# Kernel optimization log

Measured on AMD Instinct MI355X. Metric: run time of the kernel, lower is better.

## Reference

```python
import jax, jax.numpy as jnp
import numpy as np

B, T, D = 8, 512, 64

def setup_inputs() -> dict:
    key = jax.random.key(0)
    kx, kw, kb = jax.random.split(key, 3)
    x = jax.random.normal(kx, (B, T, D), dtype=jnp.float32)
    W = jax.random.normal(kw, (D, D), dtype=jnp.float32) / np.sqrt(D)
    b = jax.random.normal(kb, (D,), dtype=jnp.float32) * 0.01
    return {"x": x, "W": W, "b": b}

def reference(x, W, b):
    # v = Linear(x): (B,T,D)
    v = jnp.einsum('btd,ed->bte', x, W) + b
    # pairwise diff: (B,T,T,D); softmax over feature dim D
    diff = x[:, :, None, :] - x[:, None, :, :]
    K = jax.nn.softmax(-(diff * diff), axis=-1)
    # out[b,i,j] = sum_d K[b,i,j,d] * v[b,i,d]  -> (B,T,T)
    out = jnp.einsum('bijd,bid->bij', K, v)
    return out
```

## Files before the change

### kernel.cpp

```cpp
#include <hip/hip_runtime.h>
#include <hip/hip_bf16.h>

#define BB 8
#define TT 512
#define DD 64
#define S_SCALE 1.2011224087864498f

typedef float v2f __attribute__((ext_vector_type(2)));
typedef unsigned short ushort_t;

static __device__ __forceinline__ float fast_exp2(float v) {
#if __has_builtin(__builtin_amdgcn_exp2f)
    return __builtin_amdgcn_exp2f(v);
#else
    return exp2f(v);
#endif
}
static __device__ __forceinline__ float fast_rcp(float v) {
#if __has_builtin(__builtin_amdgcn_rcpf)
    return __builtin_amdgcn_rcpf(v);
#else
    return 1.0f / v;
#endif
}
static __device__ __forceinline__ v2f pk_fma(v2f a, v2f b, v2f c) {
#if __has_builtin(__builtin_elementwise_fma)
    return __builtin_elementwise_fma(a, b, c);
#else
    return a * b + c;
#endif
}
static __device__ __forceinline__ v2f lohi(unsigned u) {
    v2f r;
    r.x = __uint_as_float(u << 16);
    r.y = __uint_as_float(u & 0xffff0000u);
    return r;
}

__global__ __launch_bounds__(256) void rbf_pre(
    const float* __restrict__ x, const float* __restrict__ W,
    const float* __restrict__ bias, float* __restrict__ vv,
    __hip_bfloat16* __restrict__ xs16, __hip_bfloat16* __restrict__ vs16)
{
    const int t = threadIdx.x;
    const int w = t >> 6, l = t & 63;
    const int row = blockIdx.x * 4 + w;
    const float* xr = x + (size_t)row * DD;
    const float* wr = W + (size_t)l * DD;
    float acc = bias[l];
    #pragma unroll
    for (int d = 0; d < DD; d += 4) {
        float4 xv = *(const float4*)(xr + d);
        float4 wv = *(const float4*)(wr + d);
        acc = fmaf(xv.x, wv.x, acc); acc = fmaf(xv.y, wv.y, acc);
        acc = fmaf(xv.z, wv.z, acc); acc = fmaf(xv.w, wv.w, acc);
    }
    vv  [(size_t)row * DD + l] = acc;
    xs16[(size_t)row * DD + l] = __float2bfloat16(xr[l] * S_SCALE);
    vs16[(size_t)row * DD + l] = __float2bfloat16(acc);
}

template <bool MIRROR>
static __device__ __forceinline__ void tile_compute(
    const float* __restrict__ xrow0, const float* __restrict__ vrow0,
    const ushort_t* xls, const ushort_t* vls,
    float* __restrict__ orow0, float* cbuf, int l, int ilocBase)
{
    v2f nr[4][2], nc[4][2], dn[4];
    #pragma unroll
    for (int r = 0; r < 4; ++r) {
        nr[r][0] = (v2f){0.f, 0.f}; nr[r][1] = (v2f){0.f, 0.f};
        nc[r][0] = (v2f){0.f, 0.f}; nc[r][1] = (v2f){0.f, 0.f};
        dn[r]    = (v2f){0.f, 0.f};
    }
    const v2f Sv = {S_SCALE, S_SCALE};

    #pragma unroll
    for (int c = 0; c < 8; ++c) {
        uint4 xjw = *(const uint4*)(xls + l * 72 + c * 8);
        uint4 vjw = *(const uint4*)(vls + l * 72 + c * 8);
        v2f xj0 = lohi(xjw.x), xj1 = lohi(xjw.y), xj2 = lohi(xjw.z), xj3 = lohi(xjw.w);
        v2f vj0 = lohi(vjw.x), vj1 = lohi(vjw.y), vj2 = lohi(vjw.z), vj3 = lohi(vjw.w);
        #pragma unroll
        for (int r = 0; r < 4; ++r) {
            float4 a0 = *(const float4*)(xrow0 + r * DD + c * 8);
            float4 a1 = *(const float4*)(xrow0 + r * DD + c * 8 + 4);
            float4 b0 = *(const float4*)(vrow0 + r * DD + c * 8);
            float4 b1 = *(const float4*)(vrow0 + r * DD + c * 8 + 4);
            v2f u0 = pk_fma((v2f){a0.x, a0.y}, Sv, -xj0);
            v2f u1 = pk_fma((v2f){a0.z, a0.w}, Sv, -xj1);
            v2f u2 = pk_fma((v2f){a1.x, a1.y}, Sv, -xj2);
            v2f u3 = pk_fma((v2f){a1.z, a1.w}, Sv, -xj3);
            u0 *= u0; u1 *= u1; u2 *= u2; u3 *= u3;
            v2f e0 = {fast_exp2(-u0.x), fast_exp2(-u0.y)};
            v2f e1 = {fast_exp2(-u1.x), fast_exp2(-u1.y)};
            v2f e2 = {fast_exp2(-u2.x), fast_exp2(-u2.y)};
            v2f e3 = {fast_exp2(-u3.x), fast_exp2(-u3.y)};
            nr[r][0] = pk_fma(e0, (v2f){b0.x, b0.y}, nr[r][0]);
            nr[r][0] = pk_fma(e1, (v2f){b0.z, b0.w}, nr[r][0]);
            nr[r][1] = pk_fma(e2, (v2f){b1.x, b1.y}, nr[r][1]);
            nr[r][1] = pk_fma(e3, (v2f){b1.z, b1.w}, nr[r][1]);
            if (MIRROR) {
                nc[r][0] = pk_fma(e0, vj0, nc[r][0]);
                nc[r][0] = pk_fma(e1, vj1, nc[r][0]);
                nc[r][1] = pk_fma(e2, vj2, nc[r][1]);
                nc[r][1] = pk_fma(e3, vj3, nc[r][1]);
            }
            dn[r] += (e0 + e1) + (e2 + e3);
        }
    }

    #pragma unroll
    for (int r = 0; r < 4; ++r) {
        float rd = fast_rcp(dn[r].x + dn[r].y);
        v2f sr = nr[r][0] + nr[r][1];
        orow0[(size_t)r * TT + l] = (sr.x + sr.y) * rd;
        if (MIRROR) {
            v2f sc = nc[r][0] + nc[r][1];
            cbuf[l * 20 + ilocBase + r] = (sc.x + sc.y) * rd;
        }
    }
}

__global__ __launch_bounds__(256, 4) void rbf_sym(
    const float* __restrict__ x, const float* __restrict__ vv,
    const __hip_bfloat16* __restrict__ xs16, const __hip_bfloat16* __restrict__ vs16,
    float* __restrict__ out)
{
    const int bid = blockIdx.x;
    const int b = bid / 144;
    int idx = bid - b * 144;
    int st, jt, isA;
    if (idx < 32) { jt = idx >> 2; st = 4 * jt + (idx & 3); isA = 0; }
    else {
        int k = idx - 32, tt = 1;
        while (k >= 4 * tt) { k -= 4 * tt; ++tt; }
        jt = tt; st = k; isA = 1;
    }
    const int i0 = st * 16, j0 = jt * 64;

    const int tid = threadIdx.x;
    const int w = tid >> 6, l = tid & 63;
    const int wau = __builtin_amdgcn_readfirstlane(w);

    __shared__ ushort_t xls[64 * 72];
    __shared__ ushort_t vls[64 * 72];
    __shared__ float    cbuf[64 * 20];

    {
        const uint4* xsrc = (const uint4*)(xs16 + ((size_t)b * TT + j0) * DD);
        const uint4* vsrc = (const uint4*)(vs16 + ((size_t)b * TT + j0) * DD);
        #pragma unroll
        for (int u = 0; u < 2; ++u) {
            int g = u * 256 + tid;
            int r = g >> 3, c8 = g & 7;
            *(uint4*)(xls + r * 72 + c8 * 8) = xsrc[g];
            *(uint4*)(vls + r * 72 + c8 * 8) = vsrc[g];
        }
    }
    __syncthreads();

    const int ib = b * TT + i0 + wau * 4;
    const float* xrow0 = x  + (size_t)ib * DD;
    const float* vrow0 = vv + (size_t)ib * DD;
    float* outb  = out + (size_t)b * TT * TT;
    float* orow0 = outb + (size_t)(i0 + wau * 4) * TT + j0;

    if (isA) tile_compute<true >(xrow0, vrow0, xls, vls, orow0, cbuf, l, wau * 4);
    else     tile_compute<false>(xrow0, vrow0, xls, vls, orow0, cbuf, l, wau * 4);

    __syncthreads();
    if (isA) {
        int j = tid >> 2, qf = (tid & 3) * 4;
        float4 cv = *(const float4*)(cbuf + j * 20 + qf);
        *(float4*)(outb + (size_t)(j0 + j) * TT + i0 + qf) = cv;
    }
}

extern "C" void kernel_launch(void* const* d_in, const int* in_sizes, int n_in,
                              void* d_out, int out_size, void* d_ws, size_t ws_size,
                              hipStream_t stream) {
    const float* x    = (const float*)d_in[0];
    const float* W    = (const float*)d_in[1];
    const float* bias = (const float*)d_in[2];
    float* out        = (float*)d_out;

    float* vv             = (float*)d_ws;
    __hip_bfloat16* xs16  = (__hip_bfloat16*)((char*)d_ws + (1 << 20));
    __hip_bfloat16* vs16  = (__hip_bfloat16*)((char*)d_ws + (3 << 19));

    rbf_pre<<<BB * TT / 4, 256, 0, stream>>>(x, W, bias, vv, xs16, vs16);
    rbf_sym<<<BB * 144, 256, 0, stream>>>(x, vv, xs16, vs16, out);
}
```

Before: 89.51 us.

## Stage i-rows in LDS as fp16 and drop fp32 x/v global reads

Switches the precomputed scaled x and v copies from bf16 to fp16 and stops writing or reading the fp32 v buffer. The i-side rows (x pre-scaled, v) are now loaded once per block into shared memory as fp16 instead of being read per wave from global fp32 arrays. The inner loop becomes a plain subtract, because the scale is already folded in. This cuts global/L2 traffic and the per-row scale FMA, at the cost of fp16 conversions for the i operands and some reduced precision on the i side.

```diff
diff --git a/kernel.cpp b/kernel.cpp
--- a/kernel.cpp
+++ b/kernel.cpp
@@ -1,5 +1,4 @@
 #include <hip/hip_runtime.h>
-#include <hip/hip_bf16.h>
 
 #define BB 8
 #define TT 512
@@ -7,7 +6,8 @@
 #define S_SCALE 1.2011224087864498f
 
 typedef float v2f __attribute__((ext_vector_type(2)));
-typedef unsigned short ushort_t;
+typedef float f8  __attribute__((ext_vector_type(8)));
+typedef _Float16 h8 __attribute__((ext_vector_type(8)));
 
 static __device__ __forceinline__ float fast_exp2(float v) {
 #if __has_builtin(__builtin_amdgcn_exp2f)
@@ -30,17 +30,11 @@
     return a * b + c;
 #endif
 }
-static __device__ __forceinline__ v2f lohi(unsigned u) {
-    v2f r;
-    r.x = __uint_as_float(u << 16);
-    r.y = __uint_as_float(u & 0xffff0000u);
-    return r;
-}
 
 __global__ __launch_bounds__(256) void rbf_pre(
     const float* __restrict__ x, const float* __restrict__ W,
-    const float* __restrict__ bias, float* __restrict__ vv,
-    __hip_bfloat16* __restrict__ xs16, __hip_bfloat16* __restrict__ vs16)
+    const float* __restrict__ bias,
+    _Float16* __restrict__ xh, _Float16* __restrict__ vh)
 {
     const int t = threadIdx.x;
     const int w = t >> 6, l = t & 63;
@@ -55,16 +49,15 @@
         acc = fmaf(xv.x, wv.x, acc); acc = fmaf(xv.y, wv.y, acc);
         acc = fmaf(xv.z, wv.z, acc); acc = fmaf(xv.w, wv.w, acc);
     }
-    vv  [(size_t)row * DD + l] = acc;
-    xs16[(size_t)row * DD + l] = __float2bfloat16(xr[l] * S_SCALE);
-    vs16[(size_t)row * DD + l] = __float2bfloat16(acc);
+    xh[(size_t)row * DD + l] = (_Float16)(xr[l] * S_SCALE);
+    vh[(size_t)row * DD + l] = (_Float16)acc;
 }
 
 template <bool MIRROR>
 static __device__ __forceinline__ void tile_compute(
-    const float* __restrict__ xrow0, const float* __restrict__ vrow0,
-    const ushort_t* xls, const ushort_t* vls,
-    float* __restrict__ orow0, float* cbuf, int l, int ilocBase)
+    const _Float16* xls, const _Float16* vls,
+    const _Float16* xis, const _Float16* vis,
+    float* __restrict__ orow0, float* cbuf, int l, int wau)
 {
     v2f nr[4][2], nc[4][2], dn[4];
     #pragma unroll
@@ -73,40 +66,32 @@
         nc[r][0] = (v2f){0.f, 0.f}; nc[r][1] = (v2f){0.f, 0.f};
         dn[r]    = (v2f){0.f, 0.f};
     }
-    const v2f Sv = {S_SCALE, S_SCALE};
 
     #pragma unroll
     for (int c = 0; c < 8; ++c) {
-        uint4 xjw = *(const uint4*)(xls + l * 72 + c * 8);
-        uint4 vjw = *(const uint4*)(vls + l * 72 + c * 8);
-        v2f xj0 = lohi(xjw.x), xj1 = lohi(xjw.y), xj2 = lohi(xjw.z), xj3 = lohi(xjw.w);
-        v2f vj0 = lohi(vjw.x), vj1 = lohi(vjw.y), vj2 = lohi(vjw.z), vj3 = lohi(vjw.w);
+        h8 xjh = *(const h8*)(xls + l * 72 + c * 8);
+        h8 vjh = *(const h8*)(vls + l * 72 + c * 8);
+        f8 xj = __builtin_convertvector(xjh, f8);
+        f8 vj = __builtin_convertvector(vjh, f8);
+        const v2f* xj2 = (const v2f*)&xj;
+        const v2f* vj2 = (const v2f*)&vj;
         #pragma unroll
         for (int r = 0; r < 4; ++r) {
-            float4 a0 = *(const float4*)(xrow0 + r * DD + c * 8);
-            float4 a1 = *(const float4*)(xrow0 + r * DD + c * 8 + 4);
-            float4 b0 = *(const float4*)(vrow0 + r * DD + c * 8);
-            float4 b1 = *(const float4*)(vrow0 + r * DD + c * 8 + 4);
-            v2f u0 = pk_fma((v2f){a0.x, a0.y}, Sv, -xj0);
-            v2f u1 = pk_fma((v2f){a0.z, a0.w}, Sv, -xj1);
-            v2f u2 = pk_fma((v2f){a1.x, a1.y}, Sv, -xj2);
-            v2f u3 = pk_fma((v2f){a1.z, a1.w}, Sv, -xj3);
-            u0 *= u0; u1 *= u1; u2 *= u2; u3 *= u3;
-            v2f e0 = {fast_exp2(-u0.x), fast_exp2(-u0.y)};
-            v2f e1 = {fast_exp2(-u1.x), fast_exp2(-u1.y)};
-            v2f e2 = {fast_exp2(-u2.x), fast_exp2(-u2.y)};
-            v2f e3 = {fast_exp2(-u3.x), fast_exp2(-u3.y)};
-            nr[r][0] = pk_fma(e0, (v2f){b0.x, b0.y}, nr[r][0]);
-            nr[r][0] = pk_fma(e1, (v2f){b0.z, b0.w}, nr[r][0]);
-            nr[r][1] = pk_fma(e2, (v2f){b1.x, b1.y}, nr[r][1]);
-            nr[r][1] = pk_fma(e3, (v2f){b1.z, b1.w}, nr[r][1]);
-            if (MIRROR) {
-                nc[r][0] = pk_fma(e0, vj0, nc[r][0]);
-                nc[r][0] = pk_fma(e1, vj1, nc[r][0]);
-                nc[r][1] = pk_fma(e2, vj2, nc[r][1]);
-                nc[r][1] = pk_fma(e3, vj3, nc[r][1]);
+            h8 xih = *(const h8*)(xis + (wau * 4 + r) * 72 + c * 8);
+            h8 vih = *(const h8*)(vis + (wau * 4 + r) * 72 + c * 8);
+            f8 xi = __builtin_convertvector(xih, f8);
+            f8 vi = __builtin_convertvector(vih, f8);
+            const v2f* xi2 = (const v2f*)&xi;
+            const v2f* vi2 = (const v2f*)&vi;
+            #pragma unroll
+            for (int q = 0; q < 4; ++q) {
+                v2f u = xi2[q] - xj2[q];
+                u *= u;
+                v2f e = {fast_exp2(-u.x), fast_exp2(-u.y)};
+                nr[r][q & 1] = pk_fma(e, vi2[q], nr[r][q & 1]);
+                if (MIRROR) nc[r][q & 1] = pk_fma(e, vj2[q], nc[r][q & 1]);
+                dn[r] += e;
             }
-            dn[r] += (e0 + e1) + (e2 + e3);
         }
     }
 
@@ -117,14 +102,13 @@
         orow0[(size_t)r * TT + l] = (sr.x + sr.y) * rd;
         if (MIRROR) {
             v2f sc = nc[r][0] + nc[r][1];
-            cbuf[l * 20 + ilocBase + r] = (sc.x + sc.y) * rd;
+            cbuf[l * 20 + wau * 4 + r] = (sc.x + sc.y) * rd;
         }
     }
 }
 
 __global__ __launch_bounds__(256, 4) void rbf_sym(
-    const float* __restrict__ x, const float* __restrict__ vv,
-    const __hip_bfloat16* __restrict__ xs16, const __hip_bfloat16* __restrict__ vs16,
+    const _Float16* __restrict__ xh, const _Float16* __restrict__ vh,
     float* __restrict__ out)
 {
     const int bid = blockIdx.x;
@@ -143,31 +127,37 @@
     const int w = tid >> 6, l = tid & 63;
     const int wau = __builtin_amdgcn_readfirstlane(w);
 
-    __shared__ ushort_t xls[64 * 72];
-    __shared__ ushort_t vls[64 * 72];
-    __shared__ float    cbuf[64 * 20];
+    __shared__ __align__(16) _Float16 xls[64 * 72];
+    __shared__ __align__(16) _Float16 vls[64 * 72];
+    __shared__ __align__(16) _Float16 xis[16 * 72];
+    __shared__ __align__(16) _Float16 vis[16 * 72];
+    __shared__ float cbuf[64 * 20];
 
     {
-        const uint4* xsrc = (const uint4*)(xs16 + ((size_t)b * TT + j0) * DD);
-        const uint4* vsrc = (const uint4*)(vs16 + ((size_t)b * TT + j0) * DD);
+        const uint4* xsrc = (const uint4*)(xh + ((size_t)b * TT + j0) * DD);
+        const uint4* vsrc = (const uint4*)(vh + ((size_t)b * TT + j0) * DD);
         #pragma unroll
         for (int u = 0; u < 2; ++u) {
             int g = u * 256 + tid;
-            int r = g >> 3, c8 = g & 7;
-            *(uint4*)(xls + r * 72 + c8 * 8) = xsrc[g];
-            *(uint4*)(vls + r * 72 + c8 * 8) = vsrc[g];
+            int r = g >> 3, c = g & 7;
+            *(uint4*)(xls + r * 72 + c * 8) = xsrc[g];
+            *(uint4*)(vls + r * 72 + c * 8) = vsrc[g];
         }
+        const uint4* isrc = (tid < 128)
+            ? (const uint4*)(xh + ((size_t)b * TT + i0) * DD)
+            : (const uint4*)(vh + ((size_t)b * TT + i0) * DD);
+        _Float16* idst = (tid < 128) ? xis : vis;
+        int g = tid & 127;
+        int r = g >> 3, c = g & 7;
+        *(uint4*)(idst + r * 72 + c * 8) = isrc[g];
     }
     __syncthreads();
 
-    const int ib = b * TT + i0 + wau * 4;
-    const float* xrow0 = x  + (size_t)ib * DD;
-    const float* vrow0 = vv + (size_t)ib * DD;
     float* outb  = out + (size_t)b * TT * TT;
     float* orow0 = outb + (size_t)(i0 + wau * 4) * TT + j0;
 
-    if (isA) tile_compute<true >(xrow0, vrow0, xls, vls, orow0, cbuf, l, wau * 4);
-    else     tile_compute<false>(xrow0, vrow0, xls, vls, orow0, cbuf, l, wau * 4);
+    if (isA) tile_compute<true >(xls, vls, xis, vis, orow0, cbuf, l, wau);
+    else     tile_compute<false>(xls, vls, xis, vis, orow0, cbuf, l, wau);
 
     __syncthreads();
     if (isA) {
@@ -185,10 +175,9 @@
     const float* bias = (const float*)d_in[2];
     float* out        = (float*)d_out;
 
-    float* vv             = (float*)d_ws;
-    __hip_bfloat16* xs16  = (__hip_bfloat16*)((char*)d_ws + (1 << 20));
-    __hip_bfloat16* vs16  = (__hip_bfloat16*)((char*)d_ws + (3 << 19));
+    _Float16* xh = (_Float16*)d_ws;
+    _Float16* vh = (_Float16*)((char*)d_ws + (1 << 19));
 
-    rbf_pre<<<BB * TT / 4, 256, 0, stream>>>(x, W, bias, vv, xs16, vs16);
-    rbf_sym<<<BB * 144, 256, 0, stream>>>(x, vv, xs16, vs16, out);
+    rbf_pre<<<BB * TT / 4, 256, 0, stream>>>(x, W, bias, xh, vh);
+    rbf_sym<<<BB * 144, 256, 0, stream>>>(xh, vh, out);
 }
```

Measured after the change: 88.67 us. Within noise of the previous version (-0.9%).
